# Optimization experiments

Hardware: AMD Instinct MI355X
Metric: run time of the kernel (lower is better)

The kernel has to match this reference:

```python
import jax, jax.numpy as jnp
import numpy as np

H = 8          # num_heads
DM = 128       # dmodel
BN_EPS = 1e-5


def _linear(x, w, b):
    # w stored as [in, out]
    return x @ w + b


def _relu_mha(q, k, v, qw, qb, kw, kb, vw, vb, ow, ob, mask):
    """TemMulHeadAtte: ReLU on projected Q/K/V, masked softmax, ReLU out-proj.
    q,k: [B,N,T,2*DM]; v: [B,N,T,DM]; mask: broadcastable to [B,N,H,T,T] or None."""
    B, N, T, _ = q.shape
    Q = jax.nn.relu(_linear(q, qw, qb)).reshape(B, N, T, H, -1)  # e = 2*DM/H
    K = jax.nn.relu(_linear(k, kw, kb)).reshape(B, N, T, H, -1)
    V = jax.nn.relu(_linear(v, vw, vb)).reshape(B, N, T, H, -1)  # d = DM/H
    scale = 1.0 / np.sqrt(Q.shape[-1]).astype(np.float32)
    scores = jnp.einsum('bnthe,bnshe->bnhts', Q, K)
    if mask is not None:
        scores = jnp.where(mask, -jnp.inf, scores)
    attn = jax.nn.softmax(scale * scores, axis=-1)  # dropout p=0 -> identity
    out = jnp.einsum('bnhts,bnshd->bnthd', attn, V).reshape(B, N, T, -1)
    return jax.nn.relu(_linear(out, ow, ob))


def setup_inputs() -> dict:
    key = jax.random.key(0)
    ks = iter(jax.random.split(key, 32))
    B, N, T = 16, 207, 24
    def w(shape, scale=0.05):
        return (jax.random.normal(next(ks), shape, dtype=jnp.float32) * scale)
    inp = {
        'x': w((B, N, T, DM), 1.0),
        'hidden': w((B, N, T, DM), 1.0),
        'tXin': w((B, N, T, DM), 1.0),
    }
    dk = 2 * DM // H * H   # 256
    dv = DM // H * H       # 128
    for pre in ('s', 't'):  # space / temporal attention params
        inp[pre + 'q_w'] = w((2 * DM, dk)); inp[pre + 'q_b'] = w((dk,))
        inp[pre + 'k_w'] = w((2 * DM, dk)); inp[pre + 'k_b'] = w((dk,))
        inp[pre + 'v_w'] = w((DM, dv));     inp[pre + 'v_b'] = w((dv,))
        inp[pre + 'o_w'] = w((dv, DM));     inp[pre + 'o_b'] = w((DM,))
    inp['gate_w'] = w((2 * DM, DM)); inp['gate_b'] = w((DM,))
    inp['bn_gamma'] = jnp.ones((DM,), jnp.float32)
    inp['bn_beta'] = jnp.zeros((DM,), jnp.float32)
    return inp


def reference(x, hidden, tXin,
              sq_w, sq_b, sk_w, sk_b, sv_w, sv_b, so_w, so_b,
              tq_w, tq_b, tk_w, tk_b, tv_w, tv_b, to_w, to_b,
              gate_w, gate_b, bn_gamma, bn_beta):
    B, N, T, E = hidden.shape
    ht = jnp.concatenate([hidden, tXin], axis=3)  # [B,N,T,2*DM]
    # spatial attention: attend over nodes (N<->T permute)
    sqk = ht.transpose(0, 2, 1, 3)        # [B,T,N,2*DM]
    sval = hidden.transpose(0, 2, 1, 3)   # [B,T,N,DM]
    spaceOut = _relu_mha(sqk, sqk, sval, sq_w, sq_b, sk_w, sk_b, sv_w, sv_b,
                         so_w, so_b, None).transpose(0, 2, 1, 3)  # [B,N,T,DM]
    # temporal attention with causal (strict upper-tri) mask
    mask = jnp.triu(jnp.ones((T, T), dtype=bool), 1)[None, None, None]
    tempOut = _relu_mha(ht, ht, hidden, tq_w, tq_b, tk_w, tk_b, tv_w, tv_b,
                        to_w, to_b, mask)  # [B,N,T,DM]
    # gate + BatchNorm2d over channel dim (training-mode batch stats, biased var)
    gi = _linear(jnp.concatenate([spaceOut, tempOut], axis=3), gate_w, gate_b)
    mean = gi.mean(axis=(0, 1, 2))
    var = gi.var(axis=(0, 1, 2))
    z = jax.nn.sigmoid((gi - mean) * jax.lax.rsqrt(var + BN_EPS) * bn_gamma + bn_beta)
    return z * spaceOut + (1.0 - z) * tempOut
```

## Files before the change

kernel.cpp:

```cpp
#include <hip/hip_runtime.h>
#include <hip/hip_bf16.h>

typedef __bf16 bf16;
typedef __bf16 bf16x8 __attribute__((ext_vector_type(8)));
typedef float f32x4 __attribute__((ext_vector_type(4)));

#define MTOT 79488
#define NDIM 207
#define TDIM 24

#define EXP2F(x) __builtin_amdgcn_exp2f(x)

__global__ void detect_dtype(const void* __restrict__ hidden, int* __restrict__ flag,
                             float* __restrict__ stats)
{
    __shared__ int cnt;
    if (threadIdx.x == 0) cnt = 0;
    stats[threadIdx.x] = 0.f;
    __syncthreads();
    const bf16* h = (const bf16*)hidden;
    int local = 0;
    for (int i = threadIdx.x; i < 4096; i += 256) {
        float v = (float)h[i];
        if (!(fabsf(v) < 1e6f)) local++;
    }
    atomicAdd(&cnt, local);
    __syncthreads();
    if (threadIdx.x == 0) *flag = (cnt > 8) ? 1 : 0;
}

__device__ inline float ld_ext(const void* p, int idx, int isF32)
{
    return isF32 ? ((const float*)p)[idx] : (float)((const bf16*)p)[idx];
}

__global__ __launch_bounds__(256) void cvt_inputs(
    const void* __restrict__ hidden, const void* __restrict__ tXin,
    bf16* __restrict__ hb, bf16* __restrict__ tb, const int* __restrict__ dtf)
{
    const int isF32 = *dtf;
    const void* src = blockIdx.y ? tXin : hidden;
    bf16* dst = blockIdx.y ? tb : hb;
    const size_t e8 = ((size_t)blockIdx.x * 256 + threadIdx.x) * 8;
    bf16x8 v;
    if (isF32) {
        f32x4 lo = *(const f32x4*)((const float*)src + e8);
        f32x4 hi = *(const f32x4*)((const float*)src + e8 + 4);
        v[0]=(bf16)lo[0]; v[1]=(bf16)lo[1]; v[2]=(bf16)lo[2]; v[3]=(bf16)lo[3];
        v[4]=(bf16)hi[0]; v[5]=(bf16)hi[1]; v[6]=(bf16)hi[2]; v[7]=(bf16)hi[3];
    } else {
        v = *(const bf16x8*)((const bf16*)src + e8);
    }
    *(bf16x8*)(dst + e8) = v;
}

__global__ __launch_bounds__(256) void prep_weights(
    const void* __restrict__ sq, const void* __restrict__ sk, const void* __restrict__ sv,
    const void* __restrict__ so, const void* __restrict__ tq, const void* __restrict__ tk,
    const void* __restrict__ tv, const void* __restrict__ to_, const void* __restrict__ gw,
    const void* __restrict__ sqb, const void* __restrict__ skb, const void* __restrict__ svb,
    const void* __restrict__ sob, const void* __restrict__ tqb, const void* __restrict__ tkb,
    const void* __restrict__ tvb, const void* __restrict__ tob, const void* __restrict__ gb,
    bf16* __restrict__ wdst, bf16* __restrict__ bdst, const int* __restrict__ dtf)
{
    const int isF32 = *dtf;
    if (blockIdx.x == 1536) {
        for (int j = threadIdx.x; j < 1664; j += 256) {
            const void* src; int i2;
            if      (j < 256)  { src = sqb; i2 = j; }
            else if (j < 512)  { src = skb; i2 = j - 256; }
            else if (j < 640)  { src = svb; i2 = j - 512; }
            else if (j < 896)  { src = tqb; i2 = j - 640; }
            else if (j < 1152) { src = tkb; i2 = j - 896; }
            else if (j < 1280) { src = tvb; i2 = j - 1152; }
            else if (j < 1408) { src = sob; i2 = j - 1280; }
            else if (j < 1536) { src = tob; i2 = j - 1408; }
            else               { src = gb;  i2 = j - 1536; }
            bdst[j] = (bf16)ld_ext(src, i2, isF32);
        }
        return;
    }
    const int e = blockIdx.x * 256 + threadIdx.x;
    float v;
    if (e < 327680) {
        int br = (e >= 163840);
        int e2 = e - br * 163840;
        int n = e2 >> 8, k = e2 & 255;
        const void* qw = br ? tq : sq;
        const void* kw = br ? tk : sk;
        const void* vw = br ? tv : sv;
        if      (n < 256) v = ld_ext(qw, k * 256 + n, isF32);
        else if (n < 512) v = ld_ext(kw, k * 256 + (n - 256), isF32);
        else              v = (k < 128) ? ld_ext(vw, k * 128 + (n - 512), isF32) : 0.f;
    } else if (e < 360448) {
        int br = (e >= 344064);
        int e2 = e - 327680 - br * 16384;
        int n = e2 >> 7, k = e2 & 127;
        v = ld_ext(br ? to_ : so, k * 128 + n, isF32);
    } else {
        int e2 = e - 360448;
        int n = e2 >> 8, k = e2 & 255;
        v = ld_ext(gw, k * 128 + n, isF32);
    }
    wdst[e] = (bf16)v;
}

__global__ __launch_bounds__(256) void gemm_bt(
    const void* __restrict__ A0v, const void* __restrict__ A1v,
    const void* __restrict__ A0bv,
    const bf16* __restrict__ Bt, const bf16* __restrict__ bias,
    bf16* __restrict__ Ca, bf16* __restrict__ Cb,
    int Nout, int Ktot, int doRelu, int aExt,
    const int* __restrict__ dtf, int pmA, int pmB,
    float* __restrict__ stats, int ntx, int mSplit)
{
    const int aF32 = aExt & *dtf;
    __shared__ bf16 smem[2 * 128 * 72];
    bf16* As = smem;
    bf16* Bs = smem + 128 * 72;
    __shared__ float lsum[128], lsq[128];
    const int tid  = threadIdx.x;
    const int wid  = tid >> 6, lane = tid & 63;
    const int wm   = (wid >> 1) * 64, wn = (wid & 1) * 64;
    const int quad = lane >> 4, l16 = lane & 15;

    int panel, n0;
    {
        const int nwg = (int)gridDim.x;
        const int lid = (int)blockIdx.x;
        const int q = nwg >> 3, r = nwg & 7;
        const int xcd = lid & 7, idx = lid >> 3;
        const int nid = (xcd < r ? xcd * (q + 1) : r * (q + 1) + (xcd - r) * q) + idx;
        panel = nid / ntx;
        n0 = (nid % ntx) * 128;
    }
    const int gB = (panel >= mSplit);
    if (gB) panel -= mSplit;
    const int m0 = panel * 128;
    const int brOff = gB ? Nout : 0;

    const int lrow = tid >> 3;
    const int lcol = (tid & 7) * 8;

    bf16x8 av[4], bv[4];
    auto loadTiles = [&](int k0) {
        const void* Ap = gB ? A0bv : ((k0 < 128) ? A0v : A1v);
        const int koff = (k0 < 128) ? k0 : k0 - 128;
        #pragma unroll
        for (int p = 0; p < 4; ++p) {
            int r = lrow + p * 32;
            if (aF32) {
                const float* Af = (const float*)Ap;
                f32x4 lo = *(const f32x4*)(Af + (size_t)(m0 + r) * 128 + koff + lcol);
                f32x4 hi = *(const f32x4*)(Af + (size_t)(m0 + r) * 128 + koff + lcol + 4);
                bf16x8 t;
                t[0]=(bf16)lo[0]; t[1]=(bf16)lo[1]; t[2]=(bf16)lo[2]; t[3]=(bf16)lo[3];
                t[4]=(bf16)hi[0]; t[5]=(bf16)hi[1]; t[6]=(bf16)hi[2]; t[7]=(bf16)hi[3];
                av[p] = t;
            } else {
                av[p] = *(const bf16x8*)((const bf16*)Ap + (size_t)(m0 + r) * 128 + koff + lcol);
            }
            bv[p] = *(const bf16x8*)(Bt + (size_t)(n0 + brOff + r) * Ktot + k0 + lcol);
        }
    };

    loadTiles(0);
    f32x4 acc[4][4] = {};

    for (int k0 = 0; k0 < Ktot; k0 += 64) {
        #pragma unroll
        for (int p = 0; p < 4; ++p) {
            int r = lrow + p * 32;
            *(bf16x8*)&As[r * 72 + lcol] = av[p];
            *(bf16x8*)&Bs[r * 72 + lcol] = bv[p];
        }
        __syncthreads();
        if (k0 + 64 < Ktot) loadTiles(k0 + 64);
        #pragma unroll
        for (int kk = 0; kk < 64; kk += 32) {
            bf16x8 af[4], bfr[4];
            #pragma unroll
            for (int i = 0; i < 4; ++i)
                af[i] = *(const bf16x8*)&As[(wm + i * 16 + l16) * 72 + kk + quad * 8];
            #pragma unroll
            for (int j = 0; j < 4; ++j)
                bfr[j] = *(const bf16x8*)&Bs[(wn + j * 16 + l16) * 72 + kk + quad * 8];
            #pragma unroll
            for (int i = 0; i < 4; ++i)
                #pragma unroll
                for (int j = 0; j < 4; ++j)
                    acc[i][j] = __builtin_amdgcn_mfma_f32_16x16x32_bf16(
                        af[i], bfr[j], acc[i][j], 0, 0, 0);
        }
        __syncthreads();
    }

    bf16* Cp = gB ? Cb : Ca;
    const int pm = gB ? pmB : pmA;

    if (stats) {
        if (tid < 128) { lsum[tid] = 0.f; lsq[tid] = 0.f; }
        __syncthreads();
    }
    #pragma unroll
    for (int j = 0; j < 4; ++j) {
        int col = n0 + brOff + wn + j * 16 + l16;
        float bv2 = (float)bias[col];
        float ps = 0.f, psq = 0.f;
        #pragma unroll
        for (int i = 0; i < 4; ++i) {
            #pragma unroll
            for (int r = 0; r < 4; ++r) {
                float v = acc[i][j][r] + bv2;
                if (doRelu) v = fmaxf(v, 0.f);
                if (stats) { ps += v; psq += v * v; }
                acc[i][j][r] = v;
            }
        }
        if (stats) {
            atomicAdd(&lsum[col & 127], ps);
            atomicAdd(&lsq[col & 127], psq);
        }
    }

    bf16* Cs = smem;
    #pragma unroll
    for (int j = 0; j < 4; ++j)
        #pragma unroll
        for (int i = 0; i < 4; ++i)
            #pragma unroll
            for (int r = 0; r < 4; ++r)
                Cs[(wm + i * 16 + quad * 4 + r) * 132 + wn + j * 16 + l16]
                    = (bf16)acc[i][j][r];
    __syncthreads();

    if (stats && tid < 128) {
        atomicAdd(&stats[tid], lsum[tid]);
        atomicAdd(&stats[128 + tid], lsq[tid]);
    }

    const int srow = tid >> 4, scol = (tid & 15) * 8;
    #pragma unroll
    for (int pass = 0; pass < 8; ++pass) {
        int rl = pass * 16 + srow;
        int m = m0 + rl;
        int o;
        if (pm == 1) {
            int t = m % 24, bn = m / 24;
            int n = bn % 207, b = bn / 207;
            o = (b * 24 + t) * 207 + n;
        } else if (pm == 2) {
            int n = m % 207, bt = m / 207;
            int t = bt % 24, b = bt / 24;
            o = (b * 207 + n) * 24 + t;
        } else {
            o = m;
        }
        bf16x8 v = *(const bf16x8*)&Cs[rl * 132 + scol];
        *(bf16x8*)&Cp[(size_t)o * Nout + n0 + scol] = v;
    }
}

__global__ __launch_bounds__(256) void attn_spatial_mfma(
    const bf16* __restrict__ QKV, bf16* __restrict__ O)
{
    const int hh = blockIdx.x, t = blockIdx.y, b = blockIdx.z;
    __shared__ bf16 Ks[208 * 40];
    __shared__ bf16 Vt[16 * 232];
    __shared__ bf16 Pl[4][16 * 40];
    const int tid = threadIdx.x;
    const int wave = tid >> 6, lane = tid & 63;
    const int quad = lane >> 4, l16 = lane & 15;
    const size_t R = (size_t)(b * TDIM + t) * NDIM;

    for (int idx = tid; idx < 832; idx += 256) {
        int n = idx >> 2, seg = (idx & 3) * 8;
        bf16x8 v8 = {};
        if (n < NDIM)
            v8 = *(const bf16x8*)(QKV + (R + n) * 640 + 256 + hh * 32 + seg);
        *(bf16x8*)&Ks[n * 40 + seg] = v8;
    }
    for (int idx = tid; idx < 448; idx += 256) {
        int s = idx >> 1, half = (idx & 1) * 8;
        bf16x8 v8 = {};
        if (s < NDIM)
            v8 = *(const bf16x8*)(QKV + (R + s) * 640 + 512 + hh * 16 + half);
        #pragma unroll
        for (int j = 0; j < 8; ++j)
            Vt[(half + j) * 232 + s] = v8[j];
    }
    __syncthreads();

    const float k2 = 0.25506538410868237f;

    for (int qt = wave; qt < 13; qt += 4) {
        const int q0 = qt * 16;
        int qrow = q0 + l16; if (qrow >= NDIM) qrow = NDIM - 1;
        bf16x8 qfrag = *(const bf16x8*)(QKV + (R + qrow) * 640 + hh * 32 + quad * 8);
        f32x4 s[13];
        #pragma unroll
        for (int c = 0; c < 13; ++c) {
            bf16x8 kf = *(const bf16x8*)&Ks[(c * 16 + l16) * 40 + quad * 8];
            f32x4 z = {};
            s[c] = __builtin_amdgcn_mfma_f32_16x16x32_bf16(qfrag, kf, z, 0, 0, 0);
        }
        float linv[4];
        #pragma unroll
        for (int r = 0; r < 4; ++r) {
            float sum = 0.f;
            #pragma unroll
            for (int c = 0; c < 13; ++c) {
                float p = EXP2F(s[c][r] * k2);
                if (c == 12 && l16 == 15) p = 0.f;
                s[c][r] = p;
                sum += p;
            }
            sum += __shfl_xor(sum, 1);
            sum += __shfl_xor(sum, 2);
            sum += __shfl_xor(sum, 4);
            sum += __shfl_xor(sum, 8);
            linv[r] = __builtin_amdgcn_rcpf(sum);
        }
        f32x4 oacc = {};
        #pragma unroll
        for (int sc = 0; sc < 7; ++sc) {
            bf16* pb = &Pl[wave][0];
            #pragma unroll
            for (int r = 0; r < 4; ++r) {
                float p1 = 0.f;
                if (sc < 6) p1 = s[2 * sc + 1][r];
                pb[(quad * 4 + r) * 40 + l16]      = (bf16)s[2 * sc][r];
                pb[(quad * 4 + r) * 40 + 16 + l16] = (bf16)p1;
            }
            bf16x8 pf = *(const bf16x8*)&pb[l16 * 40 + quad * 8];
            bf16x8 vf = *(const bf16x8*)&Vt[l16 * 232 + sc * 32 + quad * 8];
            oacc = __builtin_amdgcn_mfma_f32_16x16x32_bf16(pf, vf, oacc, 0, 0, 0);
        }
        #pragma unroll
        for (int r = 0; r < 4; ++r) {
            int row = q0 + quad * 4 + r;
            if (row < NDIM)
                O[(R + row) * 128 + hh * 16 + l16] = (bf16)(oacc[r] * linv[r]);
        }
    }
}

__global__ __launch_bounds__(256) void attn_temporal_mfma(
    const bf16* __restrict__ QKV, bf16* __restrict__ O)
{
    const size_t m0 = (size_t)blockIdx.x * TDIM;
    __shared__ bf16 Khs[8 * 32 * 40];
    __shared__ bf16 Vts[8 * 16 * 40];
    __shared__ bf16 Pl[4][2][16 * 40];
    const int tid = threadIdx.x;
    const int wave = tid >> 6, lane = tid & 63;
    const int quad = lane >> 4, l16 = lane & 15;
    const int STR = 640;

    for (int idx = tid; idx < 32 * 32; idx += 256) {
        int row = idx >> 5, seg = idx & 31;
        int h = seg >> 2, j = (seg & 3) * 8;
        bf16x8 v8 = {};
        if (row < TDIM)
            v8 = *(const bf16x8*)(QKV + (m0 + row) * STR + 256 + h * 32 + j);
        *(bf16x8*)&Khs[h * 1280 + row * 40 + j] = v8;
    }
    for (int idx = tid; idx < 32 * 128; idx += 256) {
        int s = idx >> 7, c = idx & 127;
        int h = c >> 4, d = c & 15;
        bf16 v = (bf16)0.f;
        if (s < TDIM) v = QKV[(m0 + s) * STR + 512 + h * 16 + d];
        Vts[h * 640 + d * 40 + s] = v;
    }
    __syncthreads();

    const float k2 = 0.25506538410868237f;

    #pragma unroll
    for (int hi = 0; hi < 2; ++hi) {
        const int h = wave * 2 + hi;
        #pragma unroll
        for (int qt = 0; qt < 2; ++qt) {
            int qrow = qt * 16 + l16; if (qrow >= TDIM) qrow = TDIM - 1;
            bf16x8 qfrag = *(const bf16x8*)(QKV + (m0 + qrow) * STR + h * 32 + quad * 8);
            bf16x8 kf0 = *(const bf16x8*)&Khs[h * 1280 + l16 * 40 + quad * 8];
            bf16x8 kf1 = *(const bf16x8*)&Khs[h * 1280 + (16 + l16) * 40 + quad * 8];
            f32x4 z = {};
            f32x4 s0 = __builtin_amdgcn_mfma_f32_16x16x32_bf16(qfrag, kf0, z, 0, 0, 0);
            f32x4 s1 = __builtin_amdgcn_mfma_f32_16x16x32_bf16(qfrag, kf1, z, 0, 0, 0);
            bf16* pb = &Pl[wave][qt][0];
            float linv[4];
            #pragma unroll
            for (int r = 0; r < 4; ++r) {
                int q = qt * 16 + quad * 4 + r;
                float p0 = (l16 <= q)      ? EXP2F(s0[r] * k2) : 0.f;
                float p1 = (16 + l16 <= q) ? EXP2F(s1[r] * k2) : 0.f;
                float sum = p0 + p1;
                sum += __shfl_xor(sum, 1);
                sum += __shfl_xor(sum, 2);
                sum += __shfl_xor(sum, 4);
                sum += __shfl_xor(sum, 8);
                linv[r] = __builtin_amdgcn_rcpf(sum);
                pb[(quad * 4 + r) * 40 + l16]      = (bf16)p0;
                pb[(quad * 4 + r) * 40 + 16 + l16] = (bf16)p1;
            }
            bf16x8 pf = *(const bf16x8*)&pb[l16 * 40 + quad * 8];
            bf16x8 vf = *(const bf16x8*)&Vts[h * 640 + l16 * 40 + quad * 8];
            f32x4 oacc = __builtin_amdgcn_mfma_f32_16x16x32_bf16(pf, vf, z, 0, 0, 0);
            #pragma unroll
            for (int r = 0; r < 4; ++r) {
                int row = qt * 16 + quad * 4 + r;
                if (row < TDIM)
                    O[(m0 + row) * 128 + h * 16 + l16] = (bf16)(oacc[r] * linv[r]);
            }
        }
    }
}

__global__ __launch_bounds__(256) void bn_final(
    const bf16* __restrict__ gi, const bf16* __restrict__ sp, const bf16* __restrict__ tp,
    const void* __restrict__ gammav, const void* __restrict__ betav,
    const float* __restrict__ stats, void* __restrict__ outv,
    const int* __restrict__ dtf)
{
    const int isF32 = *dtf;
    const size_t base = ((size_t)blockIdx.x * 256 + threadIdx.x) * 8;
    const int c0 = (int)(base & 127);
    const float invM = 1.f / (float)MTOT;
    bf16x8 g8 = *(const bf16x8*)(gi + base);
    bf16x8 s8 = *(const bf16x8*)(sp + base);
    bf16x8 t8 = *(const bf16x8*)(tp + base);
    float res[8];
    #pragma unroll
    for (int j = 0; j < 8; ++j) {
        int c = c0 + j;
        float mean = stats[c] * invM;
        float var  = stats[128 + c] * invM - mean * mean;
        float gam = ld_ext(gammav, c, isF32);
        float bet = ld_ext(betav, c, isF32);
        float g = (float)g8[j];
        float zn = (g - mean) * rsqrtf(var + 1e-5f) * gam + bet;
        float z = 1.f / (1.f + EXP2F(zn * -1.4426950408889634f));
        float sv = (float)s8[j], tv = (float)t8[j];
        res[j] = z * sv + (1.f - z) * tv;
    }
    if (isF32) {
        float* op = (float*)outv + base;
        f32x4 lo = {res[0], res[1], res[2], res[3]};
        f32x4 hi = {res[4], res[5], res[6], res[7]};
        *(f32x4*)op = lo;
        *(f32x4*)(op + 4) = hi;
    } else {
        bf16x8 o8;
        #pragma unroll
        for (int j = 0; j < 8; ++j) o8[j] = (bf16)res[j];
        *(bf16x8*)((bf16*)outv + base) = o8;
    }
}

extern "C" void kernel_launch(void* const* d_in, const int* in_sizes, int n_in,
                              void* d_out, int out_size, void* d_ws, size_t ws_size,
                              hipStream_t stream)
{
    const void* hidden = d_in[1];
    const void* tXin   = d_in[2];
    const void* sq_w = d_in[3];  const void* sq_b = d_in[4];
    const void* sk_w = d_in[5];  const void* sk_b = d_in[6];
    const void* sv_w = d_in[7];  const void* sv_b = d_in[8];
    const void* so_w = d_in[9];  const void* so_b = d_in[10];
    const void* tq_w = d_in[11]; const void* tq_b = d_in[12];
    const void* tk_w = d_in[13]; const void* tk_b = d_in[14];
    const void* tv_w = d_in[15]; const void* tv_b = d_in[16];
    const void* to_w = d_in[17]; const void* to_b = d_in[18];
    const void* gate_w = d_in[19]; const void* gate_b = d_in[20];
    const void* gamma  = d_in[21]; const void* beta   = d_in[22];

    char* ws = (char*)d_ws;
    float* stats = (float*)ws;
    int*  dtf    = (int*)(ws + 1024);
    bf16* bB     = (bf16*)(ws + 2048);
    bf16* wT     = (bf16*)(ws + 8192);
    bf16* spaceO = (bf16*)(ws + 794624);
    bf16* attnOs = (bf16*)(ws + 21143552);
    bf16* QKVs   = (bf16*)(ws + 41492480);
    bf16* hb     = (bf16*)(ws + 143237120);
    bf16* tb     = (bf16*)(ws + 163586048);
    bf16* attnOt = (bf16*)(ws + 183934976);
    bf16* gi     = QKVs;

    const int tier = (ws_size >= 204283904ull) ? 2
                   : (ws_size >= 183934976ull) ? 1 : 0;
    if (tier < 2) attnOt = attnOs;
    bf16* tempO = attnOt;
    bf16* sW  = wT;            bf16* tW  = wT + 163840;
    bf16* soT = wT + 327680;   bf16* toT = wT + 344064;
    bf16* gwT = wT + 360448;
    const int BIG = 1 << 28;

    detect_dtype<<<1, 256, 0, stream>>>(hidden, dtf, stats);
    prep_weights<<<dim3(1537), 256, 0, stream>>>(
        sq_w, sk_w, sv_w, so_w, tq_w, tk_w, tv_w, to_w, gate_w,
        sq_b, sk_b, sv_b, so_b, tq_b, tk_b, tv_b, to_b, gate_b,
        wT, bB, dtf);
    if (tier >= 1)
        cvt_inputs<<<dim3(4968, 2), 256, 0, stream>>>(hidden, tXin, hb, tb, dtf);

    const void* A0 = (tier >= 1) ? (const void*)hb : hidden;
    const void* A1 = (tier >= 1) ? (const void*)tb : tXin;
    const int aExt = (tier >= 1) ? 0 : 1;

    gemm_bt<<<dim3(3105), 256, 0, stream>>>(
        A0, A1, nullptr, sW, bB, QKVs, nullptr,
        640, 256, 1, aExt, dtf, 1, 0, nullptr, 5, BIG);
    attn_spatial_mfma<<<dim3(8, TDIM, 16), 256, 0, stream>>>(QKVs, attnOs);
    if (tier < 2) {
        gemm_bt<<<dim3(621), 256, 0, stream>>>(
            attnOs, nullptr, nullptr, soT, bB + 1280, spaceO, nullptr,
            128, 128, 1, 0, dtf, 2, 0, nullptr, 1, BIG);
    }

    gemm_bt<<<dim3(3105), 256, 0, stream>>>(
        A0, A1, nullptr, tW, bB + 640, QKVs, nullptr,
        640, 256, 1, aExt, dtf, 0, 0, nullptr, 5, BIG);
    attn_temporal_mfma<<<dim3(16 * NDIM), 256, 0, stream>>>(QKVs, attnOt);

    if (tier >= 2) {
        gemm_bt<<<dim3(1242), 256, 0, stream>>>(
            attnOs, nullptr, attnOt, soT, bB + 1280, spaceO, tempO,
            128, 128, 1, 0, dtf, 2, 0, nullptr, 1, 621);
    } else {
        gemm_bt<<<dim3(621), 256, 0, stream>>>(
            attnOt, nullptr, nullptr, toT, bB + 1408, tempO, nullptr,
            128, 128, 1, 0, dtf, 0, 0, nullptr, 1, BIG);
    }

    gemm_bt<<<dim3(621), 256, 0, stream>>>(
        spaceO, tempO, nullptr, gwT, bB + 1536, gi, nullptr,
        128, 256, 0, 0, dtf, 0, 0, stats, 1, BIG);
    bn_final<<<dim3(4968), 256, 0, stream>>>(gi, spaceO, tempO, gamma, beta, stats, d_out, dtf);
}
```

Measured before the change: 489.0 us.

## Fuse spatial and temporal attention into one launch with split temporal heads

Adds a workspace tier that keeps separate spatial and temporal QKV buffers, so both attention passes run in a single combined kernel launch after both projection GEMMs. The temporal attention kernel is split into two blocks per sequence, each handling four heads with one head per wave, which doubles the grid and halves per-block shared memory staging. The aim is to cut launch and tail overhead and to raise occupancy and balance across CUs. The cost is a larger workspace requirement and a shared memory allocation sized for the larger spatial body in the fused kernel.

```diff
diff --git a/kernel.cpp b/kernel.cpp
--- a/kernel.cpp
+++ b/kernel.cpp
@@ -261,13 +261,13 @@
     }
 }
 
-__global__ __launch_bounds__(256) void attn_spatial_mfma(
-    const bf16* __restrict__ QKV, bf16* __restrict__ O)
-{
-    const int hh = blockIdx.x, t = blockIdx.y, b = blockIdx.z;
-    __shared__ bf16 Ks[208 * 40];
-    __shared__ bf16 Vt[16 * 232];
-    __shared__ bf16 Pl[4][16 * 40];
+__device__ __forceinline__ void attn_spatial_body(
+    const bf16* __restrict__ QKV, bf16* __restrict__ O,
+    int hh, int t, int b, bf16* sm)
+{
+    bf16* Ks = sm;
+    bf16* Vt = sm + 8320;
+    bf16* Pl = sm + 12032;
     const int tid = threadIdx.x;
     const int wave = tid >> 6, lane = tid & 63;
     const int quad = lane >> 4, l16 = lane & 15;
@@ -324,7 +324,7 @@
         f32x4 oacc = {};
         #pragma unroll
         for (int sc = 0; sc < 7; ++sc) {
-            bf16* pb = &Pl[wave][0];
+            bf16* pb = &Pl[wave * 640];
             #pragma unroll
             for (int r = 0; r < 4; ++r) {
                 float p1 = 0.f;
@@ -345,76 +345,101 @@
     }
 }
 
-__global__ __launch_bounds__(256) void attn_temporal_mfma(
-    const bf16* __restrict__ QKV, bf16* __restrict__ O)
-{
-    const size_t m0 = (size_t)blockIdx.x * TDIM;
-    __shared__ bf16 Khs[8 * 32 * 40];
-    __shared__ bf16 Vts[8 * 16 * 40];
-    __shared__ bf16 Pl[4][2][16 * 40];
+__device__ __forceinline__ void attn_temporal_body(
+    const bf16* __restrict__ QKV, bf16* __restrict__ O,
+    int bn, int hgrp, bf16* sm)
+{
+    bf16* Khs = sm;
+    bf16* Vts = sm + 5120;
+    bf16* Pl  = sm + 7680;
+    const size_t m0 = (size_t)bn * TDIM;
     const int tid = threadIdx.x;
     const int wave = tid >> 6, lane = tid & 63;
     const int quad = lane >> 4, l16 = lane & 15;
-    const int STR = 640;
-
-    for (int idx = tid; idx < 32 * 32; idx += 256) {
-        int row = idx >> 5, seg = idx & 31;
-        int h = seg >> 2, j = (seg & 3) * 8;
+    const int h = hgrp * 4 + wave;
+
+    for (int idx = tid; idx < 512; idx += 256) {
+        int row = idx >> 4, seg = idx & 15;
+        int hl = seg >> 2, j = (seg & 3) * 8;
         bf16x8 v8 = {};
         if (row < TDIM)
-            v8 = *(const bf16x8*)(QKV + (m0 + row) * STR + 256 + h * 32 + j);
-        *(bf16x8*)&Khs[h * 1280 + row * 40 + j] = v8;
-    }
-    for (int idx = tid; idx < 32 * 128; idx += 256) {
-        int s = idx >> 7, c = idx & 127;
-        int h = c >> 4, d = c & 15;
+            v8 = *(const bf16x8*)(QKV + (m0 + row) * 640 + 256 + (hgrp * 4 + hl) * 32 + j);
+        *(bf16x8*)&Khs[hl * 1280 + row * 40 + j] = v8;
+    }
+    for (int idx = tid; idx < 2048; idx += 256) {
+        int s = idx >> 6, c = idx & 63;
+        int hl = c >> 4, d = c & 15;
         bf16 v = (bf16)0.f;
-        if (s < TDIM) v = QKV[(m0 + s) * STR + 512 + h * 16 + d];
-        Vts[h * 640 + d * 40 + s] = v;
+        if (s < TDIM) v = QKV[(m0 + s) * 640 + 512 + (hgrp * 4 + hl) * 16 + d];
+        Vts[hl * 640 + d * 40 + s] = v;
     }
     __syncthreads();
 
     const float k2 = 0.25506538410868237f;
 
     #pragma unroll
-    for (int hi = 0; hi < 2; ++hi) {
-        const int h = wave * 2 + hi;
-        #pragma unroll
-        for (int qt = 0; qt < 2; ++qt) {
-            int qrow = qt * 16 + l16; if (qrow >= TDIM) qrow = TDIM - 1;
-            bf16x8 qfrag = *(const bf16x8*)(QKV + (m0 + qrow) * STR + h * 32 + quad * 8);
-            bf16x8 kf0 = *(const bf16x8*)&Khs[h * 1280 + l16 * 40 + quad * 8];
-            bf16x8 kf1 = *(const bf16x8*)&Khs[h * 1280 + (16 + l16) * 40 + quad * 8];
-            f32x4 z = {};
-            f32x4 s0 = __builtin_amdgcn_mfma_f32_16x16x32_bf16(qfrag, kf0, z, 0, 0, 0);
-            f32x4 s1 = __builtin_amdgcn_mfma_f32_16x16x32_bf16(qfrag, kf1, z, 0, 0, 0);
-            bf16* pb = &Pl[wave][qt][0];
-            float linv[4];
-            #pragma unroll
-            for (int r = 0; r < 4; ++r) {
-                int q = qt * 16 + quad * 4 + r;
-                float p0 = (l16 <= q)      ? EXP2F(s0[r] * k2) : 0.f;
-                float p1 = (16 + l16 <= q) ? EXP2F(s1[r] * k2) : 0.f;
-                float sum = p0 + p1;
-                sum += __shfl_xor(sum, 1);
-                sum += __shfl_xor(sum, 2);
-                sum += __shfl_xor(sum, 4);
-                sum += __shfl_xor(sum, 8);
-                linv[r] = __builtin_amdgcn_rcpf(sum);
-                pb[(quad * 4 + r) * 40 + l16]      = (bf16)p0;
-                pb[(quad * 4 + r) * 40 + 16 + l16] = (bf16)p1;
-            }
-            bf16x8 pf = *(const bf16x8*)&pb[l16 * 40 + quad * 8];
-            bf16x8 vf = *(const bf16x8*)&Vts[h * 640 + l16 * 40 + quad * 8];
-            f32x4 oacc = __builtin_amdgcn_mfma_f32_16x16x32_bf16(pf, vf, z, 0, 0, 0);
-            #pragma unroll
-            for (int r = 0; r < 4; ++r) {
-                int row = qt * 16 + quad * 4 + r;
-                if (row < TDIM)
-                    O[(m0 + row) * 128 + h * 16 + l16] = (bf16)(oacc[r] * linv[r]);
-            }
-        }
-    }
+    for (int qt = 0; qt < 2; ++qt) {
+        int qrow = qt * 16 + l16; if (qrow >= TDIM) qrow = TDIM - 1;
+        bf16x8 qfrag = *(const bf16x8*)(QKV + (m0 + qrow) * 640 + h * 32 + quad * 8);
+        bf16x8 kf0 = *(const bf16x8*)&Khs[wave * 1280 + l16 * 40 + quad * 8];
+        bf16x8 kf1 = *(const bf16x8*)&Khs[wave * 1280 + (16 + l16) * 40 + quad * 8];
+        f32x4 z = {};
+        f32x4 s0 = __builtin_amdgcn_mfma_f32_16x16x32_bf16(qfrag, kf0, z, 0, 0, 0);
+        f32x4 s1 = __builtin_amdgcn_mfma_f32_16x16x32_bf16(qfrag, kf1, z, 0, 0, 0);
+        bf16* pb = &Pl[(wave * 2 + qt) * 640];
+        float linv[4];
+        #pragma unroll
+        for (int r = 0; r < 4; ++r) {
+            int q = qt * 16 + quad * 4 + r;
+            float p0 = (l16 <= q)      ? EXP2F(s0[r] * k2) : 0.f;
+            float p1 = (16 + l16 <= q) ? EXP2F(s1[r] * k2) : 0.f;
+            float sum = p0 + p1;
+            sum += __shfl_xor(sum, 1);
+            sum += __shfl_xor(sum, 2);
+            sum += __shfl_xor(sum, 4);
+            sum += __shfl_xor(sum, 8);
+            linv[r] = __builtin_amdgcn_rcpf(sum);
+            pb[(quad * 4 + r) * 40 + l16]      = (bf16)p0;
+            pb[(quad * 4 + r) * 40 + 16 + l16] = (bf16)p1;
+        }
+        bf16x8 pf = *(const bf16x8*)&pb[l16 * 40 + quad * 8];
+        bf16x8 vf = *(const bf16x8*)&Vts[wave * 640 + l16 * 40 + quad * 8];
+        f32x4 oacc = __builtin_amdgcn_mfma_f32_16x16x32_bf16(pf, vf, z, 0, 0, 0);
+        #pragma unroll
+        for (int r = 0; r < 4; ++r) {
+            int row = qt * 16 + quad * 4 + r;
+            if (row < TDIM)
+                O[(m0 + row) * 128 + h * 16 + l16] = (bf16)(oacc[r] * linv[r]);
+        }
+    }
+}
+
+__global__ __launch_bounds__(256) void attn_fused(
+    const bf16* __restrict__ QKVs, const bf16* __restrict__ QKVt,
+    bf16* __restrict__ Os, bf16* __restrict__ Ot)
+{
+    __shared__ bf16 sm[14592];
+    const int bx = blockIdx.x;
+    if (bx < 6624) {
+        attn_temporal_body(QKVt, Ot, bx >> 1, bx & 1, sm);
+    } else {
+        int s = bx - 6624;
+        attn_spatial_body(QKVs, Os, s & 7, (s >> 3) % 24, s / 192, sm);
+    }
+}
+
+__global__ __launch_bounds__(256) void attn_spatial_mfma(
+    const bf16* __restrict__ QKV, bf16* __restrict__ O)
+{
+    __shared__ bf16 sm[14592];
+    attn_spatial_body(QKV, O, blockIdx.x, blockIdx.y, blockIdx.z, sm);
+}
+
+__global__ __launch_bounds__(256) void attn_temporal_mfma(
+    const bf16* __restrict__ QKV, bf16* __restrict__ O)
+{
+    __shared__ bf16 sm[12800];
+    attn_temporal_body(QKV, O, blockIdx.x >> 1, blockIdx.x & 1, sm);
 }
 
 __global__ __launch_bounds__(256) void bn_final(
@@ -481,6 +506,50 @@
     bf16* bB     = (bf16*)(ws + 2048);
     bf16* wT     = (bf16*)(ws + 8192);
     bf16* spaceO = (bf16*)(ws + 794624);
+
+    bf16* sW  = wT;            bf16* tW  = wT + 163840;
+    bf16* soT = wT + 327680;   bf16* toT = wT + 344064;
+    bf16* gwT = wT + 360448;
+    const int BIG = 1 << 28;
+
+    detect_dtype<<<1, 256, 0, stream>>>(hidden, dtf, stats);
+    prep_weights<<<dim3(1537), 256, 0, stream>>>(
+        sq_w, sk_w, sv_w, so_w, tq_w, tk_w, tv_w, to_w, gate_w,
+        sq_b, sk_b, sv_b, so_b, tq_b, tk_b, tv_b, to_b, gate_b,
+        wT, bB, dtf);
+
+    if (ws_size >= 265330688ull) {
+        bf16* QKVs   = (bf16*)(ws + 21143552);
+        bf16* QKVt   = (bf16*)(ws + 122888192);
+        bf16* hb     = (bf16*)(ws + 224632832);
+        bf16* tb     = (bf16*)(ws + 244981760);
+        bf16* attnOs = hb;
+        bf16* attnOt = tb;
+        bf16* tempO  = attnOt;
+        bf16* gi     = QKVs;
+
+        cvt_inputs<<<dim3(4968, 2), 256, 0, stream>>>(hidden, tXin, hb, tb, dtf);
+
+        gemm_bt<<<dim3(3105), 256, 0, stream>>>(
+            hb, tb, nullptr, sW, bB, QKVs, nullptr,
+            640, 256, 1, 0, dtf, 1, 0, nullptr, 5, BIG);
+        gemm_bt<<<dim3(3105), 256, 0, stream>>>(
+            hb, tb, nullptr, tW, bB + 640, QKVt, nullptr,
+            640, 256, 1, 0, dtf, 0, 0, nullptr, 5, BIG);
+
+        attn_fused<<<dim3(9696), 256, 0, stream>>>(QKVs, QKVt, attnOs, attnOt);
+
+        gemm_bt<<<dim3(1242), 256, 0, stream>>>(
+            attnOs, nullptr, attnOt, soT, bB + 1280, spaceO, tempO,
+            128, 128, 1, 0, dtf, 2, 0, nullptr, 1, 621);
+
+        gemm_bt<<<dim3(621), 256, 0, stream>>>(
+            spaceO, tempO, nullptr, gwT, bB + 1536, gi, nullptr,
+            128, 256, 0, 0, dtf, 0, 0, stats, 1, BIG);
+        bn_final<<<dim3(4968), 256, 0, stream>>>(gi, spaceO, tempO, gamma, beta, stats, d_out, dtf);
+        return;
+    }
+
     bf16* attnOs = (bf16*)(ws + 21143552);
     bf16* QKVs   = (bf16*)(ws + 41492480);
     bf16* hb     = (bf16*)(ws + 143237120);
@@ -492,19 +561,9 @@
                    : (ws_size >= 183934976ull) ? 1 : 0;
     if (tier < 2) attnOt = attnOs;
     bf16* tempO = attnOt;
-    bf16* sW  = wT;            bf16* tW  = wT + 163840;
-    bf16* soT = wT + 327680;   bf16* toT = wT + 344064;
-    bf16* gwT = wT + 360448;
-    const int BIG = 1 << 28;
-
-    detect_dtype<<<1, 256, 0, stream>>>(hidden, dtf, stats);
-    prep_weights<<<dim3(1537), 256, 0, stream>>>(
-        sq_w, sk_w, sv_w, so_w, tq_w, tk_w, tv_w, to_w, gate_w,
-        sq_b, sk_b, sv_b, so_b, tq_b, tk_b, tv_b, to_b, gate_b,
-        wT, bB, dtf);
+
     if (tier >= 1)
         cvt_inputs<<<dim3(4968, 2), 256, 0, stream>>>(hidden, tXin, hb, tb, dtf);
-
     const void* A0 = (tier >= 1) ? (const void*)hb : hidden;
     const void* A1 = (tier >= 1) ? (const void*)tb : tXin;
     const int aExt = (tier >= 1) ? 0 : 1;
@@ -522,7 +581,7 @@
     gemm_bt<<<dim3(3105), 256, 0, stream>>>(
         A0, A1, nullptr, tW, bB + 640, QKVs, nullptr,
         640, 256, 1, aExt, dtf, 0, 0, nullptr, 5, BIG);
-    attn_temporal_mfma<<<dim3(16 * NDIM), 256, 0, stream>>>(QKVs, attnOt);
+    attn_temporal_mfma<<<dim3(2 * 16 * NDIM), 256, 0, stream>>>(QKVs, attnOt);
 
     if (tier >= 2) {
         gemm_bt<<<dim3(1242), 256, 0, stream>>>(
```

Measured after the change: 485.2 us. No clear change (-0.8%).
